# Kernel optimization log

Hardware: AMD Instinct MI355X
Metric: run time of the kernel (lower is better)

## Reference

```python
import jax, jax.numpy as jnp
import numpy as np


def setup_inputs() -> dict:
    key = jax.random.key(0)
    kq, kk, kv, km = jax.random.split(key, 4)
    B, H, S, D = 2, 16, 2048, 64
    queries = jax.random.normal(kq, (B, H, S, D), dtype=jnp.float32)
    keys = jax.random.normal(kk, (B, H, S, D), dtype=jnp.float32)
    values = jax.random.normal(kv, (B, H, S, D), dtype=jnp.float32)
    # additive binary mask (1 = masked position), broadcast over batch/heads
    mask = jax.random.randint(km, (1, 1, S, S), 0, 2, dtype=jnp.int32)
    return {"queries": queries, "keys": keys, "values": values,
            "mask": mask, "key_dim": D}


def reference(queries, keys, values, mask, key_dim):
    # scores = Q K^T / sqrt(d)   -> [B, H, S, S]
    scale = 1.0 / jnp.sqrt(jnp.asarray(key_dim, dtype=jnp.float32))
    scores = jnp.einsum('bhqd,bhkd->bhqk', queries, keys) * scale
    # additive mask: masked positions get -1e9
    scores = scores + (-1.0e9) * mask.astype(scores.dtype)
    weights = jax.nn.softmax(scores, axis=-1)
    # attention output: weights @ V -> [B, H, S, D]
    return jnp.einsum('bhqk,bhkd->bhqd', weights, values)
```

## Files before the change

### kernel.cpp

```cpp
#include <hip/hip_runtime.h>

typedef __attribute__((ext_vector_type(8))) short short8;
typedef __attribute__((ext_vector_type(4))) float floatx4;
typedef __attribute__((ext_vector_type(2))) unsigned int uint2v;

#define S_LEN 2048
#define D_HEAD 64
#define NT64 (S_LEN / 64)
#define PITCH 72
#define TP 73
#define SCALE2 0.18033688f
#define MASK_BIAS2 -2.0e9f

static __device__ __forceinline__ unsigned short f2bf(float f) {
  unsigned int x = __builtin_bit_cast(unsigned int, f);
  x += 0x7fffu + ((x >> 16) & 1u);
  return (unsigned short)(x >> 16);
}
static __device__ __forceinline__ float bf2f(unsigned short u) {
  unsigned int x = ((unsigned int)u) << 16;
  return __builtin_bit_cast(float, x);
}
static __device__ __forceinline__ short8 cvt8(const float* __restrict__ p) {
  float4 a = *(const float4*)p;
  float4 b = *(const float4*)(p + 4);
  short8 r;
  r[0] = (short)f2bf(a.x); r[1] = (short)f2bf(a.y);
  r[2] = (short)f2bf(a.z); r[3] = (short)f2bf(a.w);
  r[4] = (short)f2bf(b.x); r[5] = (short)f2bf(b.y);
  r[6] = (short)f2bf(b.z); r[7] = (short)f2bf(b.w);
  return r;
}
static __device__ __forceinline__ short8 cvt8s(const float* __restrict__ p) {
  float4 a = *(const float4*)p;
  float4 b = *(const float4*)(p + 4);
  short8 r;
  r[0] = (short)f2bf(a.x * SCALE2); r[1] = (short)f2bf(a.y * SCALE2);
  r[2] = (short)f2bf(a.z * SCALE2); r[3] = (short)f2bf(a.w * SCALE2);
  r[4] = (short)f2bf(b.x * SCALE2); r[5] = (short)f2bf(b.y * SCALE2);
  r[6] = (short)f2bf(b.z * SCALE2); r[7] = (short)f2bf(b.w * SCALE2);
  return r;
}
static __device__ __forceinline__ void cp16(const void* g, void* l) {
  __builtin_amdgcn_global_load_lds(
      (const __attribute__((address_space(1))) unsigned int*)g,
      (__attribute__((address_space(3))) unsigned int*)l, 16, 0, 0);
}
static __device__ __forceinline__ unsigned int pk2f(float a, float b) {
  const unsigned int ab = __builtin_bit_cast(unsigned int, a) + 0x8000u;
  const unsigned int bb = __builtin_bit_cast(unsigned int, b) + 0x8000u;
  return __builtin_amdgcn_perm(bb, ab, 0x07060302u);
}
static __device__ __forceinline__ void plswap32(unsigned int& a, unsigned int& b) {
#if __has_builtin(__builtin_amdgcn_permlane32_swap)
  uint2v r = __builtin_amdgcn_permlane32_swap(a, b, false, false);
  a = r[0]; b = r[1];
#else
  asm volatile("v_permlane32_swap_b32 %0, %1" : "+v"(a), "+v"(b));
#endif
}
static __device__ __forceinline__ void plswap16(unsigned int& a, unsigned int& b) {
#if __has_builtin(__builtin_amdgcn_permlane16_swap)
  uint2v r = __builtin_amdgcn_permlane16_swap(a, b, false, false);
  a = r[0]; b = r[1];
#else
  asm volatile("v_permlane16_swap_b32 %0, %1" : "+v"(a), "+v"(b));
#endif
}

__global__ __launch_bounds__(256) void prep(
    const float* __restrict__ K, const float* __restrict__ V,
    const int* __restrict__ mask,
    unsigned short* __restrict__ Kws, unsigned short* __restrict__ Vws,
    unsigned long long* __restrict__ Mb, int BH)
{
  __shared__ unsigned short t[D_HEAD * TP];
  const int tid = threadIdx.x;
  const int nbK = BH * 64;
  const int nbV = BH * 32;
  int b = blockIdx.x;

  if (b < nbK) {
    const int tt   = b * 256 + tid;
    const int bh   = tt >> 14;
    const int rem  = tt & 16383;
    const int tile = rem >> 9;
    const int n    = rem & 511;
    const int row  = n >> 3;
    const int col8 = (n & 7) ^ (row & 7);
    short8 r = cvt8(K + ((size_t)(bh * S_LEN + tile * 64 + row)) * D_HEAD + col8 * 8);
    *(short8*)(Kws + (size_t)tt * 8) = r;
    return;
  }
  b -= nbK;
  if (b < nbV) {
    const int tile = b & 31;
    const int bh   = b >> 5;
    const int s0   = tile * 64;
    const float* Vb = V + (size_t)bh * S_LEN * D_HEAD;
#pragma unroll
    for (int p = 0; p < 4; ++p) {
      const int s  = p * 16 + (tid >> 4);
      const int d0 = (tid & 15) * 4;
      float4 v = *(const float4*)(Vb + (size_t)(s0 + s) * D_HEAD + d0);
      unsigned short* dst = &t[s * TP + d0];
      dst[0] = f2bf(v.x); dst[1] = f2bf(v.y); dst[2] = f2bf(v.z); dst[3] = f2bf(v.w);
    }
    __syncthreads();
    unsigned short* Vo = Vws + ((size_t)(bh * 32 + tile)) * 4096;
#pragma unroll
    for (int p = 0; p < 2; ++p) {
      const int n    = p * 256 + tid;
      const int d    = n >> 3;
      const int col8 = (n & 7) ^ (d & 7);
      short8 r;
#pragma unroll
      for (int j = 0; j < 8; ++j) r[j] = (short)t[(col8 * 8 + j) * TP + d];
      *(short8*)(Vo + (size_t)n * 8) = r;
    }
    return;
  }
  b -= nbV;
  const int rg   = b >> 2;
  const int cq   = b & 3;
  const int lane = tid & 63;
  const int row  = rg * 4 + (tid >> 6);
#pragma unroll 8
  for (int c = cq * 8; c < cq * 8 + 8; ++c) {
    const int mv = mask[(size_t)row * S_LEN + c * 64 + lane];
    const unsigned long long bm = __ballot(mv != 0);
    if (lane == 0) Mb[(size_t)row * NT64 + c] = bm;
  }
}

__global__ __launch_bounds__(256, 4) void fa_fwd10(
    const float* __restrict__ Q,
    const unsigned short* __restrict__ Kws,
    const unsigned short* __restrict__ Vws,
    const unsigned long long* __restrict__ Mb,
    float* __restrict__ Out)
{
  __shared__ unsigned short Kbuf[2][64 * 64];
  __shared__ unsigned short Vbuf[2][64 * 64];

  const int tid  = threadIdx.x;
  const int wv   = tid >> 6;
  const int lane = tid & 63;
  const int quad = lane >> 4;
  const int l16  = lane & 15;
  const int l8   = l16 & 7;

  const int nwg  = gridDim.x;
  const int flat = blockIdx.x;
  const int swz  = (flat & 7) * (nwg >> 3) + (flat >> 3);
  const int bh   = swz >> 5;
  const int qw   = (swz & 31) * 64 + wv * 16;

  const float* Qb = Q + (size_t)bh * S_LEN * D_HEAD;
  const unsigned short* KT = Kws + (size_t)bh * NT64 * 4096;
  const unsigned short* VT = Vws + (size_t)bh * NT64 * 4096;

  auto stage = [&](int kt, int buf) {
#pragma unroll
    for (int j = 0; j < 2; ++j) {
      const int c0 = (wv * 2 + j) * 64;
      cp16(KT + (size_t)kt * 4096 + (size_t)(c0 + lane) * 8, &Kbuf[buf][c0 * 8]);
      cp16(VT + (size_t)kt * 4096 + (size_t)(c0 + lane) * 8, &Vbuf[buf][c0 * 8]);
    }
  };

  stage(0, 0);

  short8 qfrag[2];
#pragma unroll
  for (int w = 0; w < 2; ++w)
    qfrag[w] = cvt8s(Qb + (size_t)(qw + l16) * D_HEAD + w * 32 + quad * 8);

  short8 kones;
#pragma unroll
  for (int j = 0; j < 8; ++j) kones[j] = (short)0x3F80;

  floatx4 ot[4];
#pragma unroll
  for (int dt = 0; dt < 4; ++dt) ot[dt] = (floatx4){0.f, 0.f, 0.f, 0.f};
  floatx4 lacc = (floatx4){0.f, 0.f, 0.f, 0.f};

  const unsigned long long* mrow = Mb + (size_t)(qw + l16) * NT64;

  __syncthreads();

  for (int kt = 0; kt < NT64; ++kt) {
    const int cur = kt & 1;
    if (kt + 1 < NT64) stage(kt + 1, cur ^ 1);
    const unsigned short* Kl = Kbuf[cur];
    const unsigned short* Vl = Vbuf[cur];

    floatx4 st[4];
#pragma unroll
    for (int nt = 0; nt < 4; ++nt) st[nt] = (floatx4){0.f, 0.f, 0.f, 0.f};
    __builtin_amdgcn_s_setprio(1);
#pragma unroll
    for (int w = 0; w < 2; ++w)
#pragma unroll
      for (int nt = 0; nt < 4; ++nt) {
        short8 kf = *(const short8*)&Kl[(nt * 16 + l16) * 64 + (((w * 4 + quad) ^ l8) * 8)];
        st[nt] = __builtin_amdgcn_mfma_f32_16x16x32_bf16(kf, qfrag[w], st[nt], 0, 0, 0);
      }
    __builtin_amdgcn_s_setprio(0);

    const unsigned long long mw = mrow[kt];
    unsigned int Wk[4][2];
#pragma unroll
    for (int nt = 0; nt < 4; ++nt) {
      const unsigned nib = (unsigned)(mw >> (nt * 16 + quad * 4)) & 0xFu;
      float p[4];
#pragma unroll
      for (int r = 0; r < 4; ++r) {
        float pv = __builtin_amdgcn_exp2f(st[nt][r]);
        p[r] = ((nib >> r) & 1u) ? 0.0f : pv;
      }
      Wk[nt][0] = pk2f(p[0], p[1]);
      Wk[nt][1] = pk2f(p[2], p[3]);
    }
    short8 pf[2];
#pragma unroll
    for (int w = 0; w < 2; ++w) {
      unsigned a0 = Wk[2 * w][0], b0 = Wk[2 * w + 1][0];
      plswap32(a0, b0);
      plswap16(a0, b0);
      unsigned a1 = Wk[2 * w][1], b1 = Wk[2 * w + 1][1];
      plswap32(a1, b1);
      plswap16(a1, b1);
      uint4 wd;
      wd.x = a0; wd.y = a1; wd.z = b0; wd.w = b1;
      pf[w] = __builtin_bit_cast(short8, wd);
    }

    __builtin_amdgcn_s_setprio(1);
#pragma unroll
    for (int w = 0; w < 2; ++w) {
      lacc = __builtin_amdgcn_mfma_f32_16x16x32_bf16(kones, pf[w], lacc, 0, 0, 0);
#pragma unroll
      for (int dt = 0; dt < 4; ++dt) {
        short8 vf = *(const short8*)&Vl[(dt * 16 + l16) * 64 + (((w * 4 + quad) ^ l8) * 8)];
        ot[dt] = __builtin_amdgcn_mfma_f32_16x16x32_bf16(vf, pf[w], ot[dt], 0, 0, 0);
      }
    }
    __builtin_amdgcn_s_setprio(0);

    __syncthreads();
  }

  const float invl = 1.0f / lacc[0];
  float* Ob = Out + (size_t)bh * S_LEN * D_HEAD + (size_t)(qw + l16) * D_HEAD;
#pragma unroll
  for (int dt = 0; dt < 4; ++dt) {
    float4 v;
    v.x = ot[dt][0] * invl; v.y = ot[dt][1] * invl;
    v.z = ot[dt][2] * invl; v.w = ot[dt][3] * invl;
    *(float4*)(Ob + dt * 16 + quad * 4) = v;
  }
}

__global__ __launch_bounds__(256) void fa_fwd(
    const float* __restrict__ Q, const float* __restrict__ K, const float* __restrict__ V,
    const int* __restrict__ mask, float* __restrict__ Out)
{
  __shared__ unsigned short Vt[D_HEAD * PITCH];
  __shared__ unsigned short Plds[4][16 * PITCH];
  const int tid = threadIdx.x, wv = tid >> 6, lane = tid & 63, quad = lane >> 4, l16 = lane & 15;
  const int bh = blockIdx.y, qw = blockIdx.x * 64 + wv * 16;
  const float* Qb = Q + (size_t)bh * S_LEN * D_HEAD;
  const float* Kb = K + (size_t)bh * S_LEN * D_HEAD;
  const float* Vb = V + (size_t)bh * S_LEN * D_HEAD;
  short8 qfrag[2];
#pragma unroll
  for (int w = 0; w < 2; ++w)
    qfrag[w] = cvt8(Qb + (size_t)(qw + l16) * D_HEAD + w * 32 + quad * 8);
  floatx4 o[4];
#pragma unroll
  for (int nt = 0; nt < 4; ++nt) o[nt] = (floatx4){0.f, 0.f, 0.f, 0.f};
  float m_run[4], l_run[4];
#pragma unroll
  for (int r = 0; r < 4; ++r) { m_run[r] = -1.0e30f; l_run[r] = 0.f; }
  unsigned short* pl = &Plds[wv][0];
  for (int kt = 0; kt < NT64; ++kt) {
    const int k0 = kt * 64;
    __syncthreads();
#pragma unroll
    for (int it = 0; it < 2; ++it) {
      const int s = it * 32 + (tid >> 3), d0 = (tid & 7) * 8, dblk = (tid & 7);
      const int swz = (((s >> 3) ^ dblk) & 7) * 8 + (s & 7);
      const float* vp = Vb + (size_t)(k0 + s) * D_HEAD + d0;
      float4 a = *(const float4*)vp; float4 bb = *(const float4*)(vp + 4);
      const float vvv[8] = {a.x, a.y, a.z, a.w, bb.x, bb.y, bb.z, bb.w};
#pragma unroll
      for (int j = 0; j < 8; ++j) Vt[(d0 + j) * PITCH + swz] = f2bf(vvv[j]);
    }
    __syncthreads();
    floatx4 scf[4];
#pragma unroll
    for (int nt = 0; nt < 4; ++nt) scf[nt] = (floatx4){0.f, 0.f, 0.f, 0.f};
#pragma unroll
    for (int w = 0; w < 2; ++w)
#pragma unroll
      for (int nt = 0; nt < 4; ++nt) {
        short8 kf = cvt8(Kb + (size_t)(k0 + nt * 16 + l16) * D_HEAD + w * 32 + quad * 8);
        scf[nt] = __builtin_amdgcn_mfma_f32_16x16x32_bf16(qfrag[w], kf, scf[nt], 0, 0, 0);
      }
    float s_val[4][4], mloc[4] = {-1.0e30f, -1.0e30f, -1.0e30f, -1.0e30f};
#pragma unroll
    for (int nt = 0; nt < 4; ++nt)
#pragma unroll
      for (int r = 0; r < 4; ++r) {
        const int mk = mask[(size_t)(qw + quad * 4 + r) * S_LEN + (k0 + nt * 16 + l16)];
        const float sv = scf[nt][r] * SCALE2 + (mk ? MASK_BIAS2 : 0.0f);
        s_val[nt][r] = sv; mloc[r] = fmaxf(mloc[r], sv);
      }
#pragma unroll
    for (int r = 0; r < 4; ++r)
#pragma unroll
      for (int off = 1; off < 16; off <<= 1) mloc[r] = fmaxf(mloc[r], __shfl_xor(mloc[r], off));
    float alpha[4], rsum[4];
#pragma unroll
    for (int r = 0; r < 4; ++r) {
      const float mnew = fmaxf(m_run[r], mloc[r]);
      alpha[r] = exp2f(m_run[r] - mnew); m_run[r] = mnew; rsum[r] = 0.f;
    }
#pragma unroll
    for (int nt = 0; nt < 4; ++nt)
#pragma unroll
      for (int r = 0; r < 4; ++r) {
        const float p = exp2f(s_val[nt][r] - m_run[r]);
        const unsigned short ph = f2bf(p);
        rsum[r] += bf2f(ph);
        pl[(quad * 4 + r) * PITCH + nt * 16 + l16] = ph;
      }
    __syncthreads();
#pragma unroll
    for (int r = 0; r < 4; ++r) {
#pragma unroll
      for (int off = 1; off < 16; off <<= 1) rsum[r] += __shfl_xor(rsum[r], off);
      l_run[r] = l_run[r] * alpha[r] + rsum[r];
    }
#pragma unroll
    for (int nt = 0; nt < 4; ++nt)
#pragma unroll
      for (int r = 0; r < 4; ++r) o[nt][r] *= alpha[r];
#pragma unroll
    for (int w = 0; w < 2; ++w) {
      short8 af = *(const short8*)&pl[l16 * PITCH + w * 32 + quad * 8];
#pragma unroll
      for (int nt = 0; nt < 4; ++nt) {
        const int d = nt * 16 + l16, blk = ((w * 4 + quad) ^ (d >> 3)) & 7;
        short8 vf = *(const short8*)&Vt[d * PITCH + blk * 8];
        o[nt] = __builtin_amdgcn_mfma_f32_16x16x32_bf16(af, vf, o[nt], 0, 0, 0);
      }
    }
  }
  float invl[4];
#pragma unroll
  for (int r = 0; r < 4; ++r) invl[r] = 1.0f / l_run[r];
  float* Ob = Out + (size_t)bh * S_LEN * D_HEAD;
#pragma unroll
  for (int nt = 0; nt < 4; ++nt)
#pragma unroll
    for (int r = 0; r < 4; ++r)
      Ob[(size_t)(qw + quad * 4 + r) * D_HEAD + nt * 16 + l16] = o[nt][r] * invl[r];
}

extern "C" void kernel_launch(void* const* d_in, const int* in_sizes, int n_in,
                              void* d_out, int out_size, void* d_ws, size_t ws_size,
                              hipStream_t stream) {
  const float* Q = (const float*)d_in[0];
  const float* K = (const float*)d_in[1];
  const float* V = (const float*)d_in[2];
  const int* mask = (const int*)d_in[3];
  float* Out = (float*)d_out;
  const int BH = in_sizes[0] / (S_LEN * D_HEAD);
  const size_t NH = (size_t)BH * S_LEN * D_HEAD;
  const size_t nMb = (size_t)S_LEN * NT64;
  const size_t need = NH * 2 * 2 + nMb * 8;

  if (ws_size >= need) {
    unsigned short* Kws = (unsigned short*)d_ws;
    unsigned short* Vws = Kws + NH;
    unsigned long long* Mbits = (unsigned long long*)(Vws + NH);
    const int nbPrep = BH * 64 + BH * 32 + S_LEN;
    prep<<<dim3(nbPrep), 256, 0, stream>>>(K, V, mask, Kws, Vws, Mbits, BH);
    fa_fwd10<<<dim3((S_LEN / 64) * BH), 256, 0, stream>>>(Q, Kws, Vws, Mbits, Out);
  } else {
    fa_fwd<<<dim3(S_LEN / 64, BH), 256, 0, stream>>>(Q, K, V, mask, Out);
  }
}
```

Measured before the change: 162.9 us.

## Load V fragments directly from global into registers and remap workgroup order

V tiles are no longer staged through LDS. Each wave now reads its V MFMA fragments straight from the pre-swizzled global workspace into registers at the start of each iteration, which halves LDS usage and the async copy traffic. The block-to-(head, query-chunk) mapping also changes for the 1024-block case, so that blocks sharing a head are spread across the eight XCD-interleaved slots. The tradeoff is redundant global/L2 reads of V by the four waves, plus extra register pressure and exposed global latency inside the loop.

```diff
diff --git a/kernel.cpp b/kernel.cpp
--- a/kernel.cpp
+++ b/kernel.cpp
@@ -133,7 +133,7 @@
   }
 }
 
-__global__ __launch_bounds__(256, 4) void fa_fwd10(
+__global__ __launch_bounds__(256, 4) void fa_fwd11(
     const float* __restrict__ Q,
     const unsigned short* __restrict__ Kws,
     const unsigned short* __restrict__ Vws,
@@ -141,7 +141,6 @@
     float* __restrict__ Out)
 {
   __shared__ unsigned short Kbuf[2][64 * 64];
-  __shared__ unsigned short Vbuf[2][64 * 64];
 
   const int tid  = threadIdx.x;
   const int wv   = tid >> 6;
@@ -152,24 +151,30 @@
 
   const int nwg  = gridDim.x;
   const int flat = blockIdx.x;
-  const int swz  = (flat & 7) * (nwg >> 3) + (flat >> 3);
-  const int bh   = swz >> 5;
-  const int qw   = (swz & 31) * 64 + wv * 16;
+  int bh, qc;
+  if ((nwg >> 5) == 32) {
+    bh = (flat & 7) * 4 + ((flat >> 3) & 3);
+    qc = flat >> 5;
+  } else {
+    const int swz = (flat & 7) * (nwg >> 3) + (flat >> 3);
+    bh = swz >> 5;
+    qc = swz & 31;
+  }
+  const int qw = qc * 64 + wv * 16;
 
   const float* Qb = Q + (size_t)bh * S_LEN * D_HEAD;
   const unsigned short* KT = Kws + (size_t)bh * NT64 * 4096;
   const unsigned short* VT = Vws + (size_t)bh * NT64 * 4096;
 
-  auto stage = [&](int kt, int buf) {
+  auto stageK = [&](int kt, int buf) {
 #pragma unroll
     for (int j = 0; j < 2; ++j) {
       const int c0 = (wv * 2 + j) * 64;
       cp16(KT + (size_t)kt * 4096 + (size_t)(c0 + lane) * 8, &Kbuf[buf][c0 * 8]);
-      cp16(VT + (size_t)kt * 4096 + (size_t)(c0 + lane) * 8, &Vbuf[buf][c0 * 8]);
     }
   };
 
-  stage(0, 0);
+  stageK(0, 0);
 
   short8 qfrag[2];
 #pragma unroll
@@ -191,9 +196,17 @@
 
   for (int kt = 0; kt < NT64; ++kt) {
     const int cur = kt & 1;
-    if (kt + 1 < NT64) stage(kt + 1, cur ^ 1);
+
+    const unsigned short* Vg = VT + (size_t)kt * 4096;
+    short8 vfr[2][4];
+#pragma unroll
+    for (int w = 0; w < 2; ++w)
+#pragma unroll
+      for (int dt = 0; dt < 4; ++dt)
+        vfr[w][dt] = *(const short8*)&Vg[(dt * 16 + l16) * 64 + (((w * 4 + quad) ^ l8) * 8)];
+
+    if (kt + 1 < NT64) stageK(kt + 1, cur ^ 1);
     const unsigned short* Kl = Kbuf[cur];
-    const unsigned short* Vl = Vbuf[cur];
 
     floatx4 st[4];
 #pragma unroll
@@ -241,10 +254,8 @@
     for (int w = 0; w < 2; ++w) {
       lacc = __builtin_amdgcn_mfma_f32_16x16x32_bf16(kones, pf[w], lacc, 0, 0, 0);
 #pragma unroll
-      for (int dt = 0; dt < 4; ++dt) {
-        short8 vf = *(const short8*)&Vl[(dt * 16 + l16) * 64 + (((w * 4 + quad) ^ l8) * 8)];
-        ot[dt] = __builtin_amdgcn_mfma_f32_16x16x32_bf16(vf, pf[w], ot[dt], 0, 0, 0);
-      }
+      for (int dt = 0; dt < 4; ++dt)
+        ot[dt] = __builtin_amdgcn_mfma_f32_16x16x32_bf16(vfr[w][dt], pf[w], ot[dt], 0, 0, 0);
     }
     __builtin_amdgcn_s_setprio(0);
 
@@ -388,7 +399,7 @@
     unsigned long long* Mbits = (unsigned long long*)(Vws + NH);
     const int nbPrep = BH * 64 + BH * 32 + S_LEN;
     prep<<<dim3(nbPrep), 256, 0, stream>>>(K, V, mask, Kws, Vws, Mbits, BH);
-    fa_fwd10<<<dim3((S_LEN / 64) * BH), 256, 0, stream>>>(Q, Kws, Vws, Mbits, Out);
+    fa_fwd11<<<dim3((S_LEN / 64) * BH), 256, 0, stream>>>(Q, Kws, Vws, Mbits, Out);
   } else {
     fa_fwd<<<dim3(S_LEN / 64, BH), 256, 0, stream>>>(Q, K, V, mask, Out);
   }
```

Result: slower. 182.2 us (+11.9%).
